# Kernel tuning notes

Hardware: AMD Instinct MI355X
Metric: run time of the kernel (lower is better)

The kernel has to match this reference:

```python
import jax, jax.numpy as jnp
import numpy as np

B, Q, S = 4, 16384, 4
QD = FD = HD = 256
H = W = 128
OFFSET_SCALE = 0.05


def grid_sample_bilinear(feats, grid):
    # feats [B,C,H,W], grid [B,N,2] (x,y) normalized coords, align_corners=True, zeros padding
    Bb, C, Hh, Ww = feats.shape
    x = (grid[..., 0] + 1.0) * 0.5 * (Ww - 1)
    y = (grid[..., 1] + 1.0) * 0.5 * (Hh - 1)
    x0 = jnp.floor(x)
    y0 = jnp.floor(y)
    wx1 = x - x0
    wy1 = y - y0
    x0i = x0.astype(jnp.int32)
    y0i = y0.astype(jnp.int32)
    flat = feats.reshape(Bb, C, Hh * Ww)

    def corner(xi, yi, w):
        valid = ((xi >= 0) & (xi < Ww) & (yi >= 0) & (yi < Hh)).astype(feats.dtype)
        idx = jnp.clip(yi, 0, Hh - 1) * Ww + jnp.clip(xi, 0, Ww - 1)
        vals = jnp.take_along_axis(flat, idx[:, None, :], axis=2)  # [B,C,N]
        return vals * (w * valid)[:, None, :]

    return (corner(x0i, y0i, (1 - wx1) * (1 - wy1))
            + corner(x0i + 1, y0i, wx1 * (1 - wy1))
            + corner(x0i, y0i + 1, (1 - wx1) * wy1)
            + corner(x0i + 1, y0i + 1, wx1 * wy1))  # [B,C,N]


def setup_inputs() -> dict:
    key = jax.random.key(0)
    ks = jax.random.split(key, 12)
    queries = jax.random.normal(ks[0], (B, Q, QD), jnp.float32)
    ref_points = jax.random.uniform(ks[1], (B, Q, 2), jnp.float32, -0.95, 0.95)
    feature_map = jax.random.normal(ks[2], (B, FD, H, W), jnp.float32)
    valid_mask = jax.random.randint(ks[3], (B, Q), 0, 10) > 0
    s = 0.02
    Wq = jax.random.normal(ks[4], (QD, HD), jnp.float32) * s
    bq = jnp.zeros((HD,), jnp.float32)
    Wf = jax.random.normal(ks[5], (FD, HD), jnp.float32) * s  # 1x1 conv weight
    bf = jnp.zeros((HD,), jnp.float32)
    Wo = jax.random.normal(ks[6], (QD, 2 * S), jnp.float32) * s
    bo = jnp.zeros((2 * S,), jnp.float32)
    Ww = jax.random.normal(ks[7], (QD, S), jnp.float32) * s
    bw = jnp.zeros((S,), jnp.float32)
    W1 = jax.random.normal(ks[8], (2 * HD, HD), jnp.float32) * s
    b1 = jnp.zeros((HD,), jnp.float32)
    W2 = jax.random.normal(ks[9], (HD, HD), jnp.float32) * s
    b2 = jnp.zeros((HD,), jnp.float32)
    return dict(queries=queries, ref_points=ref_points, feature_map=feature_map,
                valid_mask=valid_mask, Wq=Wq, bq=bq, Wf=Wf, bf=bf, Wo=Wo, bo=bo,
                Ww=Ww, bw=bw, W1=W1, b1=b1, W2=W2, b2=b2)


def reference(queries, ref_points, feature_map, valid_mask,
              Wq, bq, Wf, bf, Wo, bo, Ww, bw, W1, b1, W2, b2):
    Bb, Qq, _ = queries.shape
    Ss = Ww.shape[1]
    Hd = Wq.shape[1]
    pq = queries @ Wq + bq                                    # [B,Q,HD]
    pf = jnp.einsum('bchw,cd->bdhw', feature_map, Wf) + bf[None, :, None, None]
    off = jnp.tanh(queries @ Wo + bo).reshape(Bb, Qq, Ss, 2) * OFFSET_SCALE
    w = jax.nn.softmax(queries @ Ww + bw, axis=-1)            # [B,Q,S]
    grid = jnp.clip(ref_points[:, :, None, :] + off, -1.2, 1.2).reshape(Bb, Qq * Ss, 2)
    sampled = grid_sample_bilinear(pf, grid)                  # [B,HD,Q*S]
    sampled = sampled.reshape(Bb, Hd, Qq, Ss).transpose(0, 2, 3, 1)  # [B,Q,S,HD]
    m = valid_mask.astype(sampled.dtype)
    sampled = sampled * m[:, :, None, None]
    w = w * m[:, :, None]
    w = w / jnp.clip(jnp.sum(w, axis=-1, keepdims=True), 1e-6, None)
    ctx = jnp.sum(sampled * w[..., None], axis=2)             # [B,Q,HD]
    ctx = ctx * m[:, :, None]
    pq = pq * m[:, :, None]
    hcat = jnp.concatenate([pq, ctx], axis=-1)                # [B,Q,2*HD]
    return jax.nn.relu(hcat @ W1 + b1) @ W2 + b2
```

## Files before the change

### kernel.cpp

```cpp
#include <hip/hip_runtime.h>
#include <hip/hip_bf16.h>
#include <math.h>


#define NQ 65536
#define OFFSET_SCALE 0.05f

typedef __bf16 bf16x8 __attribute__((ext_vector_type(8)));
typedef float f32x4 __attribute__((ext_vector_type(4)));
typedef float f32x2 __attribute__((ext_vector_type(2)));

__device__ __forceinline__ float dot4(float4 a, float4 b) {
  return a.x * b.x + a.y * b.y + a.z * b.z + a.w * b.w;
}

__device__ __forceinline__ ushort f2bf(float f) {
  union { float f; unsigned u; } v; v.f = f;
  unsigned r = v.u + 0x7FFFu + ((v.u >> 16) & 1u);
  return (ushort)(r >> 16);
}

__device__ __forceinline__ f32x2 up2(unsigned u) {
  union { unsigned u; float f; } lo, hi;
  lo.u = u << 16;
  hi.u = u & 0xFFFF0000u;
  f32x2 r = {lo.f, hi.f};
  return r;
}

__device__ __forceinline__ unsigned pkbf(f32x2 v) {
  float2 f; f.x = v[0]; f.y = v[1];
  union { __hip_bfloat162 h; unsigned u; } x;
  x.h = __float22bfloat162_rn(f);
  return x.u;
}

__device__ __forceinline__ void gload16(const void* g, void* s) {
  __builtin_amdgcn_global_load_lds(
      (const __attribute__((address_space(1))) void*)g,
      (__attribute__((address_space(3))) void*)s, 16, 0, 0);
}

__global__ void __launch_bounds__(256) k_misc(
    const float* __restrict__ fm, ushort* __restrict__ fmT,
    const float* __restrict__ Wq, const float* __restrict__ Wf,
    const float* __restrict__ W1, const float* __restrict__ W2,
    const float* __restrict__ bq, const float* __restrict__ bf,
    ushort* __restrict__ ABt, ushort* __restrict__ W2t,
    float* __restrict__ uvec, float* __restrict__ vvec,
    const float* __restrict__ queries, const int* __restrict__ valid,
    const float* __restrict__ Wo, const float* __restrict__ bo,
    const float* __restrict__ Ww, const float* __restrict__ bw,
    float* __restrict__ proj, ushort* __restrict__ qraw) {
  __shared__ ushort tile[128][70];
  const int bid = blockIdx.x;
  const int t = threadIdx.x;

  if (bid < 2048) {
    const int c0 = (bid & 3) * 64;
    const int y  = (bid >> 2) & 127;
    const int b  = bid >> 9;
#pragma unroll
    for (int rep = 0; rep < 32; ++rep) {
      const int idx = t + rep * 256;
      const int ci = idx >> 7, x = idx & 127;
      tile[x][ci] = f2bf(fm[(((size_t)(b * 256 + c0 + ci) * 128 + y) << 7) + x]);
    }
    __syncthreads();
#pragma unroll
    for (int rep = 0; rep < 8; ++rep) {
      const int idx = t + rep * 256;
      const int x = idx >> 4, cg = idx & 15;
      const ushort4 o = *(const ushort4*)&tile[x][cg * 4];
      *(ushort4*)(fmT + (((size_t)((b * 128 + y) * 128 + x)) << 8) + c0 + cg * 4) = o;
    }
  } else if (bid < 2817) {
    const int blk = bid - 2048;
    const int n = t;
    if (blk < 256) {
      float s0 = 0.f, s1 = 0.f, s2 = 0.f, s3 = 0.f;
#pragma unroll 4
      for (int j = 0; j < 256; j += 4) {
        s0 = fmaf(Wq[blk * 256 + j + 0], W1[(j + 0) * 256 + n], s0);
        s1 = fmaf(Wq[blk * 256 + j + 1], W1[(j + 1) * 256 + n], s1);
        s2 = fmaf(Wq[blk * 256 + j + 2], W1[(j + 2) * 256 + n], s2);
        s3 = fmaf(Wq[blk * 256 + j + 3], W1[(j + 3) * 256 + n], s3);
      }
      ABt[(size_t)n * 512 + blk] = f2bf((s0 + s1) + (s2 + s3));
    } else if (blk < 512) {
      const int k = blk - 256;
      float s0 = 0.f, s1 = 0.f, s2 = 0.f, s3 = 0.f;
#pragma unroll 4
      for (int j = 0; j < 256; j += 4) {
        s0 = fmaf(Wf[k * 256 + j + 0], W1[(256 + j + 0) * 256 + n], s0);
        s1 = fmaf(Wf[k * 256 + j + 1], W1[(256 + j + 1) * 256 + n], s1);
        s2 = fmaf(Wf[k * 256 + j + 2], W1[(256 + j + 2) * 256 + n], s2);
        s3 = fmaf(Wf[k * 256 + j + 3], W1[(256 + j + 3) * 256 + n], s3);
      }
      ABt[(size_t)n * 512 + 256 + k] = f2bf((s0 + s1) + (s2 + s3));
    } else if (blk == 512) {
      float su = 0.f, sv = 0.f;
      for (int j = 0; j < 256; ++j) {
        su = fmaf(bq[j], W1[j * 256 + n], su);
        sv = fmaf(bf[j], W1[(256 + j) * 256 + n], sv);
      }
      uvec[n] = su;
      vvec[n] = sv;
    } else {
      const int k = blk - 513;
      W2t[(size_t)n * 256 + k] = f2bf(W2[(size_t)k * 256 + n]);
    }
  } else {
    const int blk = bid - 2817;
    float (*sW)[260] = (float(*)[260])&tile[0][0];
    float* sb = (float*)&tile[0][0] + 12 * 260;
    for (int i = t; i < 2048; i += 256) sW[i & 7][i >> 3] = Wo[i];
    for (int i = t; i < 1024; i += 256) sW[8 + (i & 3)][i >> 2] = Ww[i];
    if (t < 8) sb[t] = bo[t];
    else if (t < 12) sb[t] = bw[t - 8];
    __syncthreads();

    const int lane = t & 63, wv = t >> 6;
    const int ql = lane >> 4, kc = lane & 15;
    const int qi = blk * 16 + wv * 4 + ql;
    const float mf = (valid[qi] != 0) ? 1.0f : 0.0f;

    float4 qv[4];
#pragma unroll
    for (int i = 0; i < 4; ++i)
      qv[i] = *(const float4*)(queries + (size_t)qi * 256 + kc * 4 + i * 64);

    float pr[12];
#pragma unroll
    for (int j = 0; j < 12; ++j) {
      float s = 0.f;
#pragma unroll
      for (int i = 0; i < 4; ++i)
        s += dot4(qv[i], *(const float4*)&sW[j][kc * 4 + i * 64]);
      pr[j] = s;
    }
#pragma unroll
    for (int m = 1; m < 16; m <<= 1) {
#pragma unroll
      for (int j = 0; j < 12; ++j) pr[j] += __shfl_xor(pr[j], m, 64);
    }
    if (kc == 0) {
      float4* pp = (float4*)(proj + (size_t)qi * 16);
      const float4 o0 = {pr[0] + sb[0], pr[1] + sb[1], pr[2] + sb[2],  pr[3] + sb[3]};
      const float4 o1 = {pr[4] + sb[4], pr[5] + sb[5], pr[6] + sb[6],  pr[7] + sb[7]};
      const float4 o2 = {pr[8] + sb[8], pr[9] + sb[9], pr[10] + sb[10], pr[11] + sb[11]};
      pp[0] = o0; pp[1] = o1; pp[2] = o2;
    }
#pragma unroll
    for (int i = 0; i < 4; ++i) {
      ushort4 h;
      h.x = f2bf(qv[i].x * mf); h.y = f2bf(qv[i].y * mf);
      h.z = f2bf(qv[i].z * mf); h.w = f2bf(qv[i].w * mf);
      *(ushort4*)(qraw + (size_t)qi * 512 + kc * 4 + i * 64) = h;
    }
  }
}

__global__ void __launch_bounds__(256) k_gather(
    const float* __restrict__ proj, const float* __restrict__ ref,
    const int* __restrict__ valid, const ushort* __restrict__ fmT,
    ushort* __restrict__ qraw, float* __restrict__ cov) {
  const int t = threadIdx.x, lane = t & 63, wv = t >> 6;
  const int qs = lane >> 4;
  const int kc = lane & 15;
  const int xcd = blockIdx.x & 7;
  const int b = xcd >> 1;
  const int p = ((blockIdx.x >> 3) << 1) | (xcd & 1);
  const ushort* fmTb = fmT + ((size_t)b << 22);

#pragma unroll 1
  for (int it = 0; it < 2; ++it) {
    const int qi = b * 16384 + it * 8192 + p * 16 + wv * 4 + qs;
    const float mf = (valid[qi] != 0) ? 1.0f : 0.0f;
    const float4 pA = *(const float4*)(proj + (size_t)qi * 16);
    const float4 pB = *(const float4*)(proj + (size_t)qi * 16 + 4);
    const float4 pC = *(const float4*)(proj + (size_t)qi * 16 + 8);
    const float rx = ref[qi * 2], ry = ref[qi * 2 + 1];

    const float po[8] = {pA.x, pA.y, pA.z, pA.w, pB.x, pB.y, pB.z, pB.w};
    float o[8];
#pragma unroll
    for (int j = 0; j < 8; ++j) {
      const float x = po[j];
      const float e = __expf(2.0f * fabsf(x));
      const float th = 1.0f - 2.0f * __builtin_amdgcn_rcpf(e + 1.0f);
      o[j] = copysignf(th, x) * OFFSET_SCALE;
    }
    float wl[4] = {pC.x, pC.y, pC.z, pC.w};
    const float wmax = fmaxf(fmaxf(wl[0], wl[1]), fmaxf(wl[2], wl[3]));
    float wsum = 0.f;
#pragma unroll
    for (int j = 0; j < 4; ++j) { wl[j] = __expf(wl[j] - wmax); wsum += wl[j]; }
    const float winv = mf * __builtin_amdgcn_rcpf(wsum);

    f32x2 acc[8] = {};
    float cv = 0.f;

#define CORN(PIXPTR, CF)                                                     \
    do {                                                                     \
      const float cfv = (CF);                                                \
      const uint4 u0 = *(const uint4*)((PIXPTR) + kc * 8);                   \
      const uint4 u1 = *(const uint4*)((PIXPTR) + kc * 8 + 128);             \
      const f32x2 c2 = {cfv, cfv};                                           \
      acc[0] += c2 * up2(u0.x); acc[1] += c2 * up2(u0.y);                    \
      acc[2] += c2 * up2(u0.z); acc[3] += c2 * up2(u0.w);                    \
      acc[4] += c2 * up2(u1.x); acc[5] += c2 * up2(u1.y);                    \
      acc[6] += c2 * up2(u1.z); acc[7] += c2 * up2(u1.w);                    \
    } while (0)

#pragma unroll
    for (int s = 0; s < 4; ++s) {
      const float wgt = wl[s] * winv;
      const float gx = fminf(fmaxf(rx + o[2 * s],     -1.2f), 1.2f);
      const float gy = fminf(fmaxf(ry + o[2 * s + 1], -1.2f), 1.2f);
      const float xf = (gx + 1.0f) * 63.5f;
      const float yf = (gy + 1.0f) * 63.5f;
      const float x0f = floorf(xf), y0f = floorf(yf);
      const float wx = xf - x0f, wy = yf - y0f;
      const int x0 = (int)x0f, y0 = (int)y0f;
      const float wx0 = ((unsigned)x0 < 128u) ? (1.0f - wx) : 0.0f;
      const float wx1 = ((unsigned)(x0 + 1) < 128u) ? wx : 0.0f;
      const float wy0 = ((unsigned)y0 < 128u) ? (wgt * (1.0f - wy)) : 0.0f;
      const float wy1 = ((unsigned)(y0 + 1) < 128u) ? (wgt * wy) : 0.0f;
      const int xc0 = min(max(x0, 0), 127), xc1 = min(max(x0 + 1, 0), 127);
      const int yc0 = min(max(y0, 0), 127), yc1 = min(max(y0 + 1, 0), 127);
      cv += (wx0 + wx1) * (wy0 + wy1);
      const ushort* r0 = fmTb + ((size_t)yc0 << 15);
      const ushort* r1 = fmTb + ((size_t)yc1 << 15);
      CORN(r0 + (xc0 << 8), wy0 * wx0);
      CORN(r0 + (xc1 << 8), wy0 * wx1);
      CORN(r1 + (xc0 << 8), wy1 * wx0);
      CORN(r1 + (xc1 << 8), wy1 * wx1);
    }
#undef CORN

    uint4 w0, w1;
    w0.x = pkbf(acc[0]); w0.y = pkbf(acc[1]); w0.z = pkbf(acc[2]); w0.w = pkbf(acc[3]);
    w1.x = pkbf(acc[4]); w1.y = pkbf(acc[5]); w1.z = pkbf(acc[6]); w1.w = pkbf(acc[7]);
    *(uint4*)(qraw + (size_t)qi * 512 + 256 + kc * 8) = w0;
    *(uint4*)(qraw + (size_t)qi * 512 + 256 + 128 + kc * 8) = w1;
    if (kc == 0) cov[qi] = cv;
  }
}

__global__ void __launch_bounds__(256, 3) k_gemm_fused(
    const ushort* __restrict__ qraw, const ushort* __restrict__ ABt,
    const ushort* __restrict__ W2t, const int* __restrict__ valid,
    const float* __restrict__ cov, const float* __restrict__ uvec,
    const float* __restrict__ vvec, const float* __restrict__ b1,
    const float* __restrict__ b2, float* __restrict__ out) {
  __shared__ ushort As[64 * 32];
  __shared__ ushort Bs[256 * 32];
  __shared__ ushort Hs[64 * 256];
  const int t = threadIdx.x;
  const int m0 = blockIdx.x * 64;
  const int wn = t >> 6, lane = t & 63;
  const int lr = lane & 15, lg = lane >> 4;

  const int srow = t >> 2;
  const int schunk = ((t & 3) ^ ((srow >> 1) & 3)) * 8;
  const int swz = (lg ^ ((lr >> 1) & 3)) * 8;

  const ushort* ag = qraw + (size_t)(m0 + srow) * 512 + schunk;
  const ushort* bg = ABt + (size_t)srow * 512 + schunk;
  ushort* la = As + t * 8;
  ushort* lb = Bs + t * 8;

  f32x4 acc[4][4] = {};

  for (int k0 = 0; k0 < 512; k0 += 32) {
    __syncthreads();
    gload16(ag + k0, la);
    gload16(bg + k0, lb);
    gload16(bg + 64 * 512 + k0, lb + 2048);
    gload16(bg + 128 * 512 + k0, lb + 4096);
    gload16(bg + 192 * 512 + k0, lb + 6144);
    __syncthreads();
    bf16x8 af[4], bfr[4];
#pragma unroll
    for (int m = 0; m < 4; ++m)
      af[m] = *(const bf16x8*)(As + (m * 16 + lr) * 32 + swz);
#pragma unroll
    for (int n = 0; n < 4; ++n)
      bfr[n] = *(const bf16x8*)(Bs + (wn * 64 + n * 16 + lr) * 32 + swz);
#pragma unroll
    for (int m = 0; m < 4; ++m)
#pragma unroll
      for (int n = 0; n < 4; ++n)
        acc[m][n] = __builtin_amdgcn_mfma_f32_16x16x32_bf16(af[m], bfr[n], acc[m][n], 0, 0, 0);
  }

  {
    float uu[4], vv[4], bb[4];
#pragma unroll
    for (int n = 0; n < 4; ++n) {
      const int col = wn * 64 + n * 16 + lr;
      uu[n] = uvec[col]; vv[n] = vvec[col]; bb[n] = b1[col];
    }
#pragma unroll
    for (int m = 0; m < 4; ++m)
#pragma unroll
      for (int j = 0; j < 4; ++j) {
        const int row = m * 16 + lg * 4 + j;
        const float mfv = valid[m0 + row] ? 1.0f : 0.0f;
        const float cvr = cov[m0 + row];
#pragma unroll
        for (int n = 0; n < 4; ++n) {
          const int col = wn * 64 + n * 16 + lr;
          float r = acc[m][n][j] + mfv * uu[n] + cvr * vv[n] + bb[n];
          r = fmaxf(r, 0.0f);
          const int slot = (col >> 3) ^ (row & 7);
          Hs[row * 256 + slot * 8 + (col & 7)] = f2bf(r);
        }
      }
  }

  const ushort* cg = W2t + (size_t)srow * 256 + schunk;
#pragma unroll
  for (int m = 0; m < 4; ++m)
#pragma unroll
    for (int n = 0; n < 4; ++n) {
      f32x4 z = {0.f, 0.f, 0.f, 0.f};
      acc[m][n] = z;
    }

  for (int k0 = 0; k0 < 256; k0 += 32) {
    __syncthreads();
    gload16(cg + k0, lb);
    gload16(cg + 64 * 256 + k0, lb + 2048);
    gload16(cg + 128 * 256 + k0, lb + 4096);
    gload16(cg + 192 * 256 + k0, lb + 6144);
    __syncthreads();
    bf16x8 af[4], bfr[4];
#pragma unroll
    for (int m = 0; m < 4; ++m) {
      const int slot = ((k0 >> 3) + lg) ^ (lr & 7);
      af[m] = *(const bf16x8*)(Hs + (m * 16 + lr) * 256 + slot * 8);
    }
#pragma unroll
    for (int n = 0; n < 4; ++n)
      bfr[n] = *(const bf16x8*)(Bs + (wn * 64 + n * 16 + lr) * 32 + swz);
#pragma unroll
    for (int m = 0; m < 4; ++m)
#pragma unroll
      for (int n = 0; n < 4; ++n)
        acc[m][n] = __builtin_amdgcn_mfma_f32_16x16x32_bf16(af[m], bfr[n], acc[m][n], 0, 0, 0);
  }

  {
    float bb[4];
#pragma unroll
    for (int n = 0; n < 4; ++n) bb[n] = b2[wn * 64 + n * 16 + lr];
#pragma unroll
    for (int m = 0; m < 4; ++m)
#pragma unroll
      for (int j = 0; j < 4; ++j) {
        const int row = m0 + m * 16 + lg * 4 + j;
#pragma unroll
        for (int n = 0; n < 4; ++n)
          out[(size_t)row * 256 + wn * 64 + n * 16 + lr] = acc[m][n][j] + bb[n];
      }
  }
}

extern "C" void kernel_launch(void* const* d_in, const int* in_sizes, int n_in,
                              void* d_out, int out_size, void* d_ws, size_t ws_size,
                              hipStream_t stream) {
  const float* queries = (const float*)d_in[0];
  const float* ref     = (const float*)d_in[1];
  const float* fm      = (const float*)d_in[2];
  const int*   valid   = (const int*)d_in[3];
  const float* Wq = (const float*)d_in[4];
  const float* bq = (const float*)d_in[5];
  const float* Wf = (const float*)d_in[6];
  const float* bf = (const float*)d_in[7];
  const float* Wo = (const float*)d_in[8];
  const float* bo = (const float*)d_in[9];
  const float* Ww = (const float*)d_in[10];
  const float* bw = (const float*)d_in[11];
  const float* W1 = (const float*)d_in[12];
  const float* b1 = (const float*)d_in[13];
  const float* W2 = (const float*)d_in[14];
  const float* b2 = (const float*)d_in[15];
  float* out = (float*)d_out;

  char* ws = (char*)d_ws;
  ushort* qraw = (ushort*)ws;
  float*  cov  = (float*)(ws + 67108864);
  ushort* ABt  = (ushort*)(ws + 67108864 + 262144);
  ushort* W2t  = (ushort*)(ws + 67108864 + 524288);
  float*  uvec = (float*)(ws + 67108864 + 655360);
  float*  vvec = uvec + 256;

  ushort* fmT  = (ushort*)d_out;
  float*  proj = out + 9437184;

  k_misc<<<6913, 256, 0, stream>>>(fm, fmT, Wq, Wf, W1, W2, bq, bf, ABt, W2t,
                                   uvec, vvec, queries, valid, Wo, bo, Ww, bw,
                                   proj, qraw);
  k_gather<<<2048, 256, 0, stream>>>(proj, ref, valid, fmT, qraw, cov);
  k_gemm_fused<<<1024, 256, 0, stream>>>(qraw, ABt, W2t, valid, cov, uvec, vvec,
                                         b1, b2, out);
}
```

Before: 136.9 us.

## Coarsen weight-fold blocks, interleave transpose and projection blocks, widen stores

The weight-folding work (Wq·W1, Wf·W1, W2 transpose) is coarsened from 769 single-column blocks to 49 blocks that each compute 16 rows, reusing each W1 load 16 times and writing 16-byte vector stores. The feature-map transpose blocks are interleaved 1:2 with the query-projection blocks so memory-heavy and compute-heavy work share the GPU concurrently rather than running in separate phases. The transpose writeout uses 8-element stores. The risk is that the 49 heavy blocks with 16 accumulators each become a long tail in the schedule.

```diff
diff --git a/kernel.cpp b/kernel.cpp
--- a/kernel.cpp
+++ b/kernel.cpp
@@ -9,6 +9,7 @@
 typedef __bf16 bf16x8 __attribute__((ext_vector_type(8)));
 typedef float f32x4 __attribute__((ext_vector_type(4)));
 typedef float f32x2 __attribute__((ext_vector_type(2)));
+typedef unsigned short u16x8 __attribute__((ext_vector_type(8)));
 
 __device__ __forceinline__ float dot4(float4 a, float4 b) {
   return a.x * b.x + a.y * b.y + a.z * b.z + a.w * b.w;
@@ -56,10 +57,55 @@
   const int bid = blockIdx.x;
   const int t = threadIdx.x;
 
-  if (bid < 2048) {
-    const int c0 = (bid & 3) * 64;
-    const int y  = (bid >> 2) & 127;
-    const int b  = bid >> 9;
+  if (bid < 49) {
+    const int n = t;
+    if (bid < 32) {
+      const int k0 = bid * 16;
+      const float* src = (bid < 16) ? (Wq + (size_t)k0 * 256)
+                                    : (Wf + (size_t)(k0 - 256) * 256);
+      const int joff = (bid < 16) ? 0 : 256;
+      float acc[16];
+#pragma unroll
+      for (int r = 0; r < 16; ++r) acc[r] = 0.f;
+#pragma unroll 4
+      for (int j = 0; j < 256; ++j) {
+        const float w = W1[(size_t)(j + joff) * 256 + n];
+#pragma unroll
+        for (int r = 0; r < 16; ++r) acc[r] = fmaf(src[r * 256 + j], w, acc[r]);
+      }
+      u16x8 o0, o1;
+#pragma unroll
+      for (int r = 0; r < 8; ++r) { o0[r] = f2bf(acc[r]); o1[r] = f2bf(acc[8 + r]); }
+      *(u16x8*)(ABt + (size_t)n * 512 + k0) = o0;
+      *(u16x8*)(ABt + (size_t)n * 512 + k0 + 8) = o1;
+    } else if (bid == 32) {
+      float su = 0.f, sv = 0.f;
+      for (int j = 0; j < 256; ++j) {
+        su = fmaf(bq[j], W1[(size_t)j * 256 + n], su);
+        sv = fmaf(bf[j], W1[(size_t)(256 + j) * 256 + n], sv);
+      }
+      uvec[n] = su;
+      vvec[n] = sv;
+    } else {
+      const int k0 = (bid - 33) * 16;
+      u16x8 o0, o1;
+#pragma unroll
+      for (int r = 0; r < 8; ++r) {
+        o0[r] = f2bf(W2[(size_t)(k0 + r) * 256 + n]);
+        o1[r] = f2bf(W2[(size_t)(k0 + 8 + r) * 256 + n]);
+      }
+      *(u16x8*)(W2t + (size_t)n * 256 + k0) = o0;
+      *(u16x8*)(W2t + (size_t)n * 256 + k0 + 8) = o1;
+    }
+    return;
+  }
+
+  const int r3 = bid - 49;
+  if ((r3 % 3) == 0) {
+    const int tb = r3 / 3;
+    const int c0 = (tb & 3) * 64;
+    const int y  = (tb >> 2) & 127;
+    const int b  = tb >> 9;
 #pragma unroll
     for (int rep = 0; rep < 32; ++rep) {
       const int idx = t + rep * 256;
@@ -68,50 +114,16 @@
     }
     __syncthreads();
 #pragma unroll
-    for (int rep = 0; rep < 8; ++rep) {
+    for (int rep = 0; rep < 4; ++rep) {
       const int idx = t + rep * 256;
-      const int x = idx >> 4, cg = idx & 15;
-      const ushort4 o = *(const ushort4*)&tile[x][cg * 4];
-      *(ushort4*)(fmT + (((size_t)((b * 128 + y) * 128 + x)) << 8) + c0 + cg * 4) = o;
-    }
-  } else if (bid < 2817) {
-    const int blk = bid - 2048;
-    const int n = t;
-    if (blk < 256) {
-      float s0 = 0.f, s1 = 0.f, s2 = 0.f, s3 = 0.f;
-#pragma unroll 4
-      for (int j = 0; j < 256; j += 4) {
-        s0 = fmaf(Wq[blk * 256 + j + 0], W1[(j + 0) * 256 + n], s0);
-        s1 = fmaf(Wq[blk * 256 + j + 1], W1[(j + 1) * 256 + n], s1);
-        s2 = fmaf(Wq[blk * 256 + j + 2], W1[(j + 2) * 256 + n], s2);
-        s3 = fmaf(Wq[blk * 256 + j + 3], W1[(j + 3) * 256 + n], s3);
-      }
-      ABt[(size_t)n * 512 + blk] = f2bf((s0 + s1) + (s2 + s3));
-    } else if (blk < 512) {
-      const int k = blk - 256;
-      float s0 = 0.f, s1 = 0.f, s2 = 0.f, s3 = 0.f;
-#pragma unroll 4
-      for (int j = 0; j < 256; j += 4) {
-        s0 = fmaf(Wf[k * 256 + j + 0], W1[(256 + j + 0) * 256 + n], s0);
-        s1 = fmaf(Wf[k * 256 + j + 1], W1[(256 + j + 1) * 256 + n], s1);
-        s2 = fmaf(Wf[k * 256 + j + 2], W1[(256 + j + 2) * 256 + n], s2);
-        s3 = fmaf(Wf[k * 256 + j + 3], W1[(256 + j + 3) * 256 + n], s3);
-      }
-      ABt[(size_t)n * 512 + 256 + k] = f2bf((s0 + s1) + (s2 + s3));
-    } else if (blk == 512) {
-      float su = 0.f, sv = 0.f;
-      for (int j = 0; j < 256; ++j) {
-        su = fmaf(bq[j], W1[j * 256 + n], su);
-        sv = fmaf(bf[j], W1[(256 + j) * 256 + n], sv);
-      }
-      uvec[n] = su;
-      vvec[n] = sv;
-    } else {
-      const int k = blk - 513;
-      W2t[(size_t)n * 256 + k] = f2bf(W2[(size_t)k * 256 + n]);
+      const int x = idx >> 3, c8 = idx & 7;
+      const ushort4 a = *(const ushort4*)&tile[x][c8 * 8];
+      const ushort4 b4 = *(const ushort4*)&tile[x][c8 * 8 + 4];
+      const u16x8 o = {a.x, a.y, a.z, a.w, b4.x, b4.y, b4.z, b4.w};
+      *(u16x8*)(fmT + (((size_t)((b * 128 + y) * 128 + x)) << 8) + c0 + c8 * 8) = o;
     }
   } else {
-    const int blk = bid - 2817;
+    const int blk = (r3 / 3) * 2 + (r3 % 3) - 1;
     float (*sW)[260] = (float(*)[260])&tile[0][0];
     float* sb = (float*)&tile[0][0] + 12 * 260;
     for (int i = t; i < 2048; i += 256) sW[i & 7][i >> 3] = Wo[i];
@@ -400,7 +412,7 @@
   ushort* fmT  = (ushort*)d_out;
   float*  proj = out + 9437184;
 
-  k_misc<<<6913, 256, 0, stream>>>(fm, fmT, Wq, Wf, W1, W2, bq, bf, ABt, W2t,
+  k_misc<<<6193, 256, 0, stream>>>(fm, fmT, Wq, Wf, W1, W2, bq, bf, ABt, W2t,
                                    uvec, vvec, queries, valid, Wo, bo, Ww, bw,
                                    proj, qraw);
   k_gather<<<2048, 256, 0, stream>>>(proj, ref, valid, fmT, qraw, cov);
```

Result: no change. 136.2 us (-0.5%).
